# Performance work log

Hardware: AMD Instinct MI355X
Metric: run time of the kernel (lower is better)

## Reference

```python
import jax, jax.numpy as jnp
import numpy as np

EPS = 1e-3  # keras BatchNormalization epsilon=0.001
CLIP = 20.0

def bn(x, g, b, m, v):
    # inference-mode batch norm over last axis
    return (x - m) * jax.lax.rsqrt(v + EPS) * g + b

def conv1d_relu(x, w, b, stride):
    # x: [B,T,C], w: [K,Cin,Cout], VALID padding, relu
    y = jax.lax.conv_general_dilated(x, w, (stride,), 'VALID',
                                     dimension_numbers=('NWC', 'WIO', 'NWC'))
    return jax.nn.relu(y + b)

def gru_dir(xp, Wh, bh, reverse):
    # xp: [B,T,3H] precomputed input projection (x@Wx + input bias)
    # keras GRU, reset_after=True, activation=relu, recurrent_activation=sigmoid
    B, T, H3 = xp.shape
    H = H3 // 3
    def step(h, xt):
        mh = h @ Wh + bh                       # [B,3H]
        xz, xr, xh = jnp.split(xt, 3, axis=-1)
        rz, rr, rh = jnp.split(mh, 3, axis=-1)
        z = jax.nn.sigmoid(xz + rz)
        r = jax.nn.sigmoid(xr + rr)
        hh = jax.nn.relu(xh + r * rh)
        h = z * h + (1.0 - z) * hh
        return h, h
    xs = jnp.swapaxes(xp, 0, 1)                # [T,B,3H]
    h0 = jnp.zeros((B, H), xp.dtype)
    _, ys = jax.lax.scan(step, h0, xs, reverse=reverse)
    return jnp.swapaxes(ys, 0, 1)              # [B,T,H]

def bi_gru_sum(x, Wx, Wh, b):
    # Wx: [2,in,3H], Wh: [2,H,3H], b: [2,2,3H] (input bias, recurrent bias)
    out = None
    for d in range(2):
        xp = x @ Wx[d] + b[d, 0]
        y = gru_dir(xp, Wh[d], b[d, 1], reverse=(d == 1))
        out = y if out is None else out + y
    return out


def setup_inputs() -> dict:
    key = jax.random.key(0)
    ks = jax.random.split(key, 16)
    B, T, F = 16, 1600, 80
    C = 512      # conv filters / gru units / fc units
    K = 5        # kernel size
    L = 3        # bi_gru layers
    V = 6000     # output_dim
    def rn(k, shape, s):
        return (jax.random.normal(k, shape, jnp.float32) * s)
    inp = {
        'x': rn(ks[0], (B, T, F), 1.0),
        'bn1_g': jnp.ones((F,), jnp.float32), 'bn1_b': jnp.zeros((F,), jnp.float32),
        'bn1_m': rn(ks[1], (F,), 0.1), 'bn1_v': jnp.ones((F,), jnp.float32),
        'conv_w0': rn(ks[2], (K, F, C), 0.05), 'conv_b0': jnp.zeros((C,), jnp.float32),
        'conv_w1': rn(ks[3], (K, C, C), 0.02), 'conv_b1': jnp.zeros((C,), jnp.float32),
        'bn2_g': jnp.ones((C,), jnp.float32), 'bn2_b': jnp.zeros((C,), jnp.float32),
        'bn2_m': rn(ks[4], (C,), 0.1), 'bn2_v': jnp.ones((C,), jnp.float32),
        # stacked GRU params: [layers, 2 dirs, ...]; relu recurrence -> small init
        'gru_wx': rn(ks[5], (L, 2, C, 3 * C), 0.03),
        'gru_wh': rn(ks[6], (L, 2, C, 3 * C), 0.03),
        'gru_b': jnp.zeros((L, 2, 2, 3 * C), jnp.float32),
        'bn3_g': jnp.ones((C,), jnp.float32), 'bn3_b': jnp.zeros((C,), jnp.float32),
        'bn3_m': rn(ks[7], (C,), 0.1), 'bn3_v': jnp.ones((C,), jnp.float32),
        'fc_w': rn(ks[8], (C, C), 0.04), 'fc_b': jnp.zeros((C,), jnp.float32),
        'sm_w': rn(ks[9], (C, V), 0.04), 'sm_b': jnp.zeros((V,), jnp.float32),
    }
    return inp


def reference(x, bn1_g, bn1_b, bn1_m, bn1_v,
              conv_w0, conv_b0, conv_w1, conv_b1,
              bn2_g, bn2_b, bn2_m, bn2_v,
              gru_wx, gru_wh, gru_b,
              bn3_g, bn3_b, bn3_m, bn3_v,
              fc_w, fc_b, sm_w, sm_b):
    x = bn(x, bn1_g, bn1_b, bn1_m, bn1_v)
    x = conv1d_relu(x, conv_w0, conv_b0, 2)    # [B,798,512]
    x = conv1d_relu(x, conv_w1, conv_b1, 2)    # [B,397,512]
    x = bn(x, bn2_g, bn2_b, bn2_m, bn2_v)
    for l in range(gru_wx.shape[0]):
        x = bi_gru_sum(x, gru_wx[l], gru_wh[l], gru_b[l])
    x = bn(x, bn3_g, bn3_b, bn3_m, bn3_v)
    x = jnp.minimum(jax.nn.relu(x @ fc_w + fc_b), CLIP)  # clipped_relu(max=20)
    return jax.nn.softmax(x @ sm_w + sm_b, axis=-1)      # [B,397,6000]
```

## Files before the change

### kernel.cpp

```cpp
#include <hip/hip_runtime.h>
#include <math.h>

using bf16x8 = __attribute__((ext_vector_type(8))) short;
using f32x4  = __attribute__((ext_vector_type(4))) float;
using u32x4  = __attribute__((ext_vector_type(4))) unsigned int;
typedef unsigned short u16;
typedef unsigned int   u32;

#define EPSBN 1e-3f

__device__ __forceinline__ u16 f2bf(float f){
  union { float f; u32 u; } c; c.f = f;
  u32 u = c.u + 0x7fffu + ((c.u >> 16) & 1u);
  return (u16)(u >> 16);
}
__device__ __forceinline__ float bf2f(u16 b){
  union { u32 u; float f; } c; c.u = ((u32)b) << 16; return c.f;
}
__device__ __forceinline__ void splitstore(float v, u16* ph, u16* pl){
  u16 h = f2bf(v); *ph = h; *pl = f2bf(v - bf2f(h));
}
__device__ __forceinline__ f32x4 MFMA(bf16x8 a, bf16x8 b, f32x4 c){
  return __builtin_amdgcn_mfma_f32_16x16x32_bf16(a, b, c, 0, 0, 0);
}
__device__ __forceinline__ void glds16(const u16* g, u16* l){
  __builtin_amdgcn_global_load_lds(
      (const __attribute__((address_space(1))) void*)g,
      (__attribute__((address_space(3))) void*)l, 16, 0, 0);
}

__device__ __forceinline__ void st32_sys(u32* p, u32 v){
  asm volatile("global_store_dword %0, %1, off sc0 sc1" :: "v"(p), "v"(v) : "memory");
}
__device__ __forceinline__ u32 ld32_sys(const u32* p){
  u32 r;
  asm volatile("global_load_dword %0, %1, off sc0 sc1\n\ts_waitcnt vmcnt(0)"
               : "=v"(r) : "v"(p) : "memory");
  return r;
}

__global__ __launch_bounds__(256) void k_bn1_split(
    const float* __restrict__ x, const float* __restrict__ g, const float* __restrict__ b,
    const float* __restrict__ m, const float* __restrict__ v,
    u16* __restrict__ oh, u16* __restrict__ ol)
{
  int i = blockIdx.x*256 + threadIdx.x;
  if (i >= 2048000) return;
  int ci = i % 80;
  float s = g[ci] * rsqrtf(v[ci] + EPSBN);
  float val = (x[i] - m[ci]) * s + b[ci];
  splitstore(val, oh+i, ol+i);
}

__global__ __launch_bounds__(256) void k_prep_c1w(
    const float* __restrict__ w0, u16* __restrict__ oh, u16* __restrict__ ol)
{
  int i = blockIdx.x*256 + threadIdx.x;
  if (i >= 512*416) return;
  int co = i / 416, kf = i - co*416;
  float val = 0.f;
  if (kf < 400){ int kw = kf/80, ci = kf - kw*80; val = w0[(kw*80+ci)*512 + co]; }
  splitstore(val, oh+i, ol+i);
}

__global__ __launch_bounds__(256) void k_prep_c2w(
    const float* __restrict__ w1, u16* __restrict__ oh, u16* __restrict__ ol)
{
  int i = blockIdx.x*256 + threadIdx.x;
  if (i >= 5*512*512) return;
  int co = i & 511, ci = (i >> 9) & 511, kw = i >> 18;
  long o = (long)co*2560 + kw*512 + ci;
  splitstore(w1[i], oh+o, ol+o);
}

__global__ __launch_bounds__(256) void k_prep_wx(
    const float* __restrict__ wx, const float* __restrict__ g2, const float* __restrict__ v2,
    u16* __restrict__ oh, u16* __restrict__ ol)
{
  long i = (long)blockIdx.x*256 + threadIdx.x;
  if (i >= 6L*512*1536) return;
  int n = (int)(i % 1536); long r2 = i / 1536; int k = (int)(r2 % 512); int ld = (int)(r2 / 512);
  float s = (ld < 2) ? g2[k]*rsqrtf(v2[k]+EPSBN) : 1.f;
  long o = ((long)ld*1536 + n)*512 + k;
  splitstore(wx[i]*s, oh+o, ol+o);
}

__global__ __launch_bounds__(256) void k_prep_wh(
    const float* __restrict__ wh, u16* __restrict__ oh, u16* __restrict__ ol)
{
  long i = (long)blockIdx.x*256 + threadIdx.x;
  if (i >= 6L*512*1536) return;
  int n = (int)(i % 1536); long r2 = i / 1536; int k = (int)(r2 % 512); int ld = (int)(r2 / 512);
  long o = ((long)ld*1536 + n)*512 + k;
  splitstore(wh[i], oh+o, ol+o);
}

__global__ __launch_bounds__(256) void k_prep_grub(
    const float* __restrict__ gb, const float* __restrict__ wx,
    const float* __restrict__ g2, const float* __restrict__ b2,
    const float* __restrict__ m2, const float* __restrict__ v2,
    float* __restrict__ xbias, float* __restrict__ hbias)
{
  int i = blockIdx.x*256 + threadIdx.x;
  if (i >= 6*1536) return;
  int n = i % 1536, ld = i / 1536;
  float xv = gb[(ld*2 + 0)*1536 + n];
  float hv = gb[(ld*2 + 1)*1536 + n];
  if (ld < 2){
    float acc = 0.f;
    for (int k = 0; k < 512; ++k){
      float s = g2[k]*rsqrtf(v2[k]+EPSBN);
      float t = b2[k] - m2[k]*s;
      acc += t * wx[((long)ld*512 + k)*1536 + n];
    }
    xv += acc;
  }
  xbias[i] = xv; hbias[i] = hv;
}

__global__ __launch_bounds__(256) void k_prep_fcw(
    const float* __restrict__ fw, const float* __restrict__ g3, const float* __restrict__ v3,
    u16* __restrict__ oh, u16* __restrict__ ol)
{
  int i = blockIdx.x*256 + threadIdx.x;
  if (i >= 512*512) return;
  int n = i & 511, k = i >> 9;
  float s = g3[k]*rsqrtf(v3[k]+EPSBN);
  long o = (long)n*512 + k;
  splitstore(fw[i]*s, oh+o, ol+o);
}

__global__ __launch_bounds__(256) void k_prep_fcb(
    const float* __restrict__ fw, const float* __restrict__ fb,
    const float* __restrict__ g3, const float* __restrict__ b3,
    const float* __restrict__ m3, const float* __restrict__ v3,
    float* __restrict__ ob)
{
  int n = blockIdx.x*256 + threadIdx.x;
  if (n >= 512) return;
  float acc = fb[n];
  for (int k = 0; k < 512; ++k){
    float s = g3[k]*rsqrtf(v3[k]+EPSBN);
    float t = b3[k] - m3[k]*s;
    acc += t * fw[k*512 + n];
  }
  ob[n] = acc;
}

__global__ __launch_bounds__(256) void k_prep_smw(
    const float* __restrict__ sw, u16* __restrict__ oh, u16* __restrict__ ol)
{
  long i = (long)blockIdx.x*256 + threadIdx.x;
  if (i >= 512L*6000) return;
  int n = (int)(i % 6000); int k = (int)(i / 6000);
  long o = (long)n*512 + k;
  splitstore(sw[i], oh+o, ol+o);
}

__global__ __launch_bounds__(256) void k_sumsplit(
    const float* __restrict__ a, const float* __restrict__ b,
    u16* __restrict__ oh, u16* __restrict__ ol)
{
  int i = blockIdx.x*256 + threadIdx.x;
  if (i >= 6352*512) return;
  splitstore(a[i] + b[i], oh+i, ol+i);
}

template<int AMODE, int EPI>
__global__ __launch_bounds__(256,1)
void gemm_split(const u16* __restrict__ Ah, const u16* __restrict__ Al,
                const u16* __restrict__ Bh, const u16* __restrict__ Bl,
                const float* __restrict__ bias,
                float* __restrict__ outF, u16* __restrict__ outH, u16* __restrict__ outL,
                int M, int N, int K, int Kvalid, int TIN, int TOUT, int NYB)
{
  constexpr int CW = (AMODE==1) ? 80 : 512;
  const int tid  = threadIdx.x;
  const int lane = tid & 63;
  const int w    = tid >> 6;
  const int wm = w >> 1, wn = w & 1;
  const int r  = lane & 15, kg = lane >> 4;

  const int nwg = gridDim.x;
  const int q   = nwg >> 3;
  const int bid = blockIdx.x;
  const int wg  = (bid & 7) * q + (bid >> 3);
  const int bx  = wg / NYB, by = wg - bx * NYB;

  const int m0 = by * 64 + wm * 32;
  const int n0 = bx * 64 + wn * 32;

  long abase[2];
  #pragma unroll
  for (int mt = 0; mt < 2; ++mt){
    int m = m0 + mt*16 + r;
    int mc = m < M ? m : M - 1;
    if (AMODE == 0) abase[mt] = (long)mc * K;
    else { int bb = mc / TOUT; int tt = mc - bb * TOUT; abase[mt] = ((long)bb * TIN + 2*tt) * CW; }
  }
  long bbase[2];
  #pragma unroll
  for (int nt = 0; nt < 2; ++nt){
    int n = n0 + nt*16 + r;
    int nc = n < N ? n : N - 1;
    bbase[nt] = (long)nc * K;
  }

  f32x4 acc[2][2];
  #pragma unroll
  for (int a_ = 0; a_ < 2; ++a_)
    #pragma unroll
    for (int b_ = 0; b_ < 2; ++b_) acc[a_][b_] = f32x4{0.f,0.f,0.f,0.f};

  const bf16x8 zfrag = {0,0,0,0,0,0,0,0};
  const int koff = kg * 8;
  const int KT = K >> 5;
  for (int kt = 0; kt < KT; ++kt){
    int kf = kt*32 + koff;
    bf16x8 ah[2], al[2], bh[2], bl[2];
    #pragma unroll
    for (int nt = 0; nt < 2; ++nt){
      bh[nt] = *(const bf16x8*)(Bh + bbase[nt] + kf);
      bl[nt] = *(const bf16x8*)(Bl + bbase[nt] + kf);
    }
    #pragma unroll
    for (int mt = 0; mt < 2; ++mt){
      if (kf < Kvalid){
        int kw = kf / CW; int ci = kf - kw*CW;
        long ao = abase[mt] + (long)kw*CW + ci;
        ah[mt] = *(const bf16x8*)(Ah + ao); al[mt] = *(const bf16x8*)(Al + ao);
      } else { ah[mt] = zfrag; al[mt] = zfrag; }
    }
    #pragma unroll
    for (int mt = 0; mt < 2; ++mt)
      #pragma unroll
      for (int nt = 0; nt < 2; ++nt){
        acc[mt][nt] = MFMA(ah[mt], bh[nt], acc[mt][nt]);
        acc[mt][nt] = MFMA(ah[mt], bl[nt], acc[mt][nt]);
        acc[mt][nt] = MFMA(al[mt], bh[nt], acc[mt][nt]);
      }
  }

  #pragma unroll
  for (int nt = 0; nt < 2; ++nt){
    int n = n0 + nt*16 + r;
    if (n >= N) continue;
    float bv = bias ? bias[n] : 0.f;
    #pragma unroll
    for (int mt = 0; mt < 2; ++mt){
      #pragma unroll
      for (int q2 = 0; q2 < 4; ++q2){
        int m = m0 + mt*16 + kg*4 + q2;
        if (m >= M) continue;
        float v = acc[mt][nt][q2] + bv;
        if (EPI == 1) v = fmaxf(v, 0.f);
        if (EPI == 2) v = fminf(fmaxf(v, 0.f), 20.f);
        long o = (long)m * N + n;
        if (EPI == 0) outF[o] = v;
        else { u16 h = f2bf(v); outH[o] = h; outL[o] = f2bf(v - bf2f(h)); }
      }
    }
  }
}

template<int AMODE, int EPI>
__global__ __launch_bounds__(256,1)
void gemm_lds(const u16* __restrict__ Ah, const u16* __restrict__ Al,
              const u16* __restrict__ Bh, const u16* __restrict__ Bl,
              const float* __restrict__ bias,
              float* __restrict__ outF, u16* __restrict__ outH, u16* __restrict__ outL,
              int M, int N, int K, int TIN, int TOUT, int NYB, int NTILES)
{
  __shared__ __align__(16) u16 sAh[128*32], sAl[128*32], sBh[128*32], sBl[128*32];

  const int tid  = threadIdx.x;
  const int lane = tid & 63;
  const int w    = tid >> 6;
  const int wm = w >> 1, wn = w & 1;
  const int r  = lane & 15, kg = lane >> 4;

  const int nwg = gridDim.x;
  const int qq  = nwg >> 3;
  const int wg  = (blockIdx.x & 7) * qq + (blockIdx.x >> 3);
  if (wg >= NTILES) return;
  const int bx  = wg / NYB, by = wg - bx * NYB;
  const int m0 = by * 128, n0 = bx * 128;

  long aoff[2], boff[2]; int cbase[2];
  #pragma unroll
  for (int cc = 0; cc < 2; ++cc){
    int c = w*2 + cc;
    int li = c*64 + lane;
    int row = li >> 2, seg = li & 3;
    cbase[cc] = c*512;
    int ma = m0 + row; if (ma >= M) ma = M - 1;
    if (AMODE == 0) aoff[cc] = (long)ma * K + seg*8;
    else { int bb = ma / TOUT; int tt = ma - bb*TOUT;
           aoff[cc] = ((long)bb * TIN + 2*tt) * 512 + seg*8; }
    int nb = n0 + row; if (nb >= N) nb = N - 1;
    boff[cc] = (long)nb * K + seg*8;
  }

  int ard[4], brd[4];
  #pragma unroll
  for (int t4 = 0; t4 < 4; ++t4){
    ard[t4] = (wm*64 + t4*16 + r)*32 + kg*8;
    brd[t4] = (wn*64 + t4*16 + r)*32 + kg*8;
  }

  f32x4 acc[4][4];
  #pragma unroll
  for (int i = 0; i < 4; ++i)
    #pragma unroll
    for (int j = 0; j < 4; ++j) acc[i][j] = f32x4{0.f,0.f,0.f,0.f};

  const int KT = K >> 5;
  for (int kt = 0; kt < KT; ++kt){
    const long k32 = (long)kt*32;
    #pragma unroll
    for (int cc = 0; cc < 2; ++cc){
      glds16(Ah + aoff[cc] + k32, sAh + cbase[cc]);
      glds16(Al + aoff[cc] + k32, sAl + cbase[cc]);
      glds16(Bh + boff[cc] + k32, sBh + cbase[cc]);
      glds16(Bl + boff[cc] + k32, sBl + cbase[cc]);
    }
    asm volatile("s_waitcnt vmcnt(0)" ::: "memory");
    __syncthreads();

    bf16x8 ah[4], al[4], bh[4], bl[4];
    #pragma unroll
    for (int t4 = 0; t4 < 4; ++t4){
      ah[t4] = *(const bf16x8*)(sAh + ard[t4]);
      al[t4] = *(const bf16x8*)(sAl + ard[t4]);
      bh[t4] = *(const bf16x8*)(sBh + brd[t4]);
      bl[t4] = *(const bf16x8*)(sBl + brd[t4]);
    }
    #pragma unroll
    for (int i = 0; i < 4; ++i)
      #pragma unroll
      for (int j = 0; j < 4; ++j){
        acc[i][j] = MFMA(ah[i], bh[j], acc[i][j]);
        acc[i][j] = MFMA(ah[i], bl[j], acc[i][j]);
        acc[i][j] = MFMA(al[i], bh[j], acc[i][j]);
      }
    __syncthreads();
  }

  #pragma unroll
  for (int j = 0; j < 4; ++j){
    int n = n0 + wn*64 + j*16 + r;
    if (n >= N) continue;
    float bv = bias ? bias[n] : 0.f;
    #pragma unroll
    for (int i = 0; i < 4; ++i){
      #pragma unroll
      for (int q2 = 0; q2 < 4; ++q2){
        int m = m0 + wm*64 + i*16 + kg*4 + q2;
        if (m >= M) continue;
        float v = acc[i][j][q2] + bv;
        if (EPI == 1) v = fmaxf(v, 0.f);
        if (EPI == 2) v = fminf(fmaxf(v, 0.f), 20.f);
        long o = (long)m * N + n;
        if (EPI == 0) outF[o] = v;
        else { u16 h = f2bf(v); outH[o] = h; outL[o] = f2bf(v - bf2f(h)); }
      }
    }
  }
}

__global__ __launch_bounds__(256,1)
void gru_layer(const float* __restrict__ xp,
               const u16* __restrict__ WhH, const u16* __restrict__ WhL,
               const float* __restrict__ hbias,
               float* __restrict__ yf, float* __restrict__ yb,
               u32* __restrict__ hq,
               u32* __restrict__ flags,
               u32 lcode)
{
  const int dir = blockIdx.x >> 5;
  const int s   = blockIdx.x & 31;
  const int tid = threadIdx.x, lane = tid & 63, w = tid >> 6;
  const int r = lane & 15, kg = lane >> 4;

  const float* xpd = xp + (long)dir * (6352L*1536);
  const u16* whh = WhH + (long)dir * (1536L*512);
  const u16* whl = WhL + (long)dir * (1536L*512);
  const float* hb = hbias + dir * 1536;
  float* y = dir ? yb : yf;
  u32* flg = flags + dir * 512;

  __shared__ float red[2][4][3][64][4];

  bf16x8 Bh[3][4], Bl[3][4];
  #pragma unroll
  for (int g = 0; g < 3; ++g){
    long nb = (long)(g*512 + s*16 + r) * 512;
    #pragma unroll
    for (int kk = 0; kk < 4; ++kk){
      int k = (w*4 + kk)*32 + kg*8;
      Bh[g][kk] = *(const bf16x8*)(whh + nb + k);
      Bl[g][kk] = *(const bf16x8*)(whl + nb + k);
    }
  }

  const int gb = tid >> 4, gj = tid & 15;
  const int gcol = s*16 + gj;
  const float bz = hb[gcol], br = hb[512 + gcol], bhh = hb[1024 + gcol];
  const int rl = ((gb >> 2) << 4) | gj;
  const int rq = gb & 3;
  float hreg = 0.f;

  for (int t = 0; t < 397; ++t){
    const int tpos = dir ? (396 - t) : t;
    const long xb_ = ((long)gb*397 + tpos)*1536 + gcol;
    float xz = xpd[xb_], xr = xpd[xb_ + 512], xh = xpd[xb_ + 1024];

    f32x4 a0 = f32x4{0.f,0.f,0.f,0.f}, a1 = a0, a2 = a0;
    if (t > 0){
      if (w == 0){
        const u32 tgt = lcode + (u32)t;
        for (;;){
          int done = 1;
          if (lane < 32) done = (ld32_sys(flg + lane*16) >= tgt);
          if (__all(done)) break;
        }
      }
      __syncthreads();

      const u32* hqs = hq + ((long)t*2 + dir) * 8192;
      const int cbase2 = r*512 + kg*8;
      u32x4 q0[4], q1[4];
      #pragma unroll
      for (int kk = 0; kk < 4; ++kk){
        const u32x4* pp = (const u32x4*)(hqs + cbase2 + (w*4 + kk)*32);
        q0[kk] = pp[0]; q1[kk] = pp[1];
      }

      bf16x8 ah[4], al[4];
      #pragma unroll
      for (int kk = 0; kk < 4; ++kk){
        union { bf16x8 v; u32 u[4]; } A, L;
        A.u[0] = __builtin_amdgcn_perm(q0[kk].y, q0[kk].x, 0x07060302u);
        L.u[0] = __builtin_amdgcn_perm(q0[kk].y, q0[kk].x, 0x05040100u);
        A.u[1] = __builtin_amdgcn_perm(q0[kk].w, q0[kk].z, 0x07060302u);
        L.u[1] = __builtin_amdgcn_perm(q0[kk].w, q0[kk].z, 0x05040100u);
        A.u[2] = __builtin_amdgcn_perm(q1[kk].y, q1[kk].x, 0x07060302u);
        L.u[2] = __builtin_amdgcn_perm(q1[kk].y, q1[kk].x, 0x05040100u);
        A.u[3] = __builtin_amdgcn_perm(q1[kk].w, q1[kk].z, 0x07060302u);
        L.u[3] = __builtin_amdgcn_perm(q1[kk].w, q1[kk].z, 0x05040100u);
        ah[kk] = A.v; al[kk] = L.v;
      }
      #pragma unroll
      for (int kk = 0; kk < 4; ++kk){
        a0 = MFMA(ah[kk], Bh[0][kk], a0); a0 = MFMA(ah[kk], Bl[0][kk], a0); a0 = MFMA(al[kk], Bh[0][kk], a0);
        a1 = MFMA(ah[kk], Bh[1][kk], a1); a1 = MFMA(ah[kk], Bl[1][kk], a1); a1 = MFMA(al[kk], Bh[1][kk], a1);
        a2 = MFMA(ah[kk], Bh[2][kk], a2); a2 = MFMA(ah[kk], Bl[2][kk], a2); a2 = MFMA(al[kk], Bh[2][kk], a2);
      }
    }
    const int tb = t & 1;
    *(f32x4*)&red[tb][w][0][lane][0] = a0;
    *(f32x4*)&red[tb][w][1][lane][0] = a1;
    *(f32x4*)&red[tb][w][2][lane][0] = a2;
    __syncthreads();
    float rz = bz, rr = br, rh = bhh;
    #pragma unroll
    for (int ww = 0; ww < 4; ++ww){
      rz += red[tb][ww][0][rl][rq];
      rr += red[tb][ww][1][rl][rq];
      rh += red[tb][ww][2][rl][rq];
    }
    float z  = 1.f / (1.f + __expf(-(xz + rz)));
    float rg = 1.f / (1.f + __expf(-(xr + rr)));
    float hh = fmaxf(xh + rg * rh, 0.f);
    hreg = z * hreg + (1.f - z) * hh;

    {
      u32* o = hq + ((long)(t+1)*2 + dir) * 8192 + gb*512 + gcol;
      u16 hi = f2bf(hreg); u16 lo = f2bf(hreg - bf2f(hi));
      st32_sys(o, ((u32)hi << 16) | (u32)lo);
    }
    asm volatile("s_waitcnt vmcnt(0)" ::: "memory");
    __syncthreads();
    if (tid == 0) st32_sys(flg + s*16, lcode + (u32)(t + 1));
    y[((long)gb*397 + tpos)*512 + gcol] = hreg;
  }
}

__global__ __launch_bounds__(256,1) void k_softmax(float* __restrict__ out)
{
  const int tid = threadIdx.x;
  float* prow = out + (long)blockIdx.x * 6000;
  float vals[24];
  float mx = -3.0e38f;
  #pragma unroll
  for (int i = 0; i < 24; ++i){
    int idx = tid + i*256;
    vals[i] = (idx < 6000) ? prow[idx] : -3.0e38f;
    mx = fmaxf(mx, vals[i]);
  }
  #pragma unroll
  for (int o = 32; o; o >>= 1) mx = fmaxf(mx, __shfl_xor(mx, o));
  __shared__ float sred[4];
  if ((tid & 63) == 0) sred[tid >> 6] = mx;
  __syncthreads();
  mx = fmaxf(fmaxf(sred[0], sred[1]), fmaxf(sred[2], sred[3]));
  __syncthreads();
  float sum = 0.f;
  #pragma unroll
  for (int i = 0; i < 24; ++i){
    int idx = tid + i*256;
    vals[i] = (idx < 6000) ? expf(vals[i] - mx) : 0.f;
    sum += vals[i];
  }
  #pragma unroll
  for (int o = 32; o; o >>= 1) sum += __shfl_xor(sum, o);
  if ((tid & 63) == 0) sred[tid >> 6] = sum;
  __syncthreads();
  sum = sred[0] + sred[1] + sred[2] + sred[3];
  float inv = 1.f / sum;
  #pragma unroll
  for (int i = 0; i < 24; ++i){
    int idx = tid + i*256;
    if (idx < 6000) prow[idx] = vals[i] * inv;
  }
}

extern "C" void kernel_launch(void* const* d_in, const int* in_sizes, int n_in,
                              void* d_out, int out_size, void* d_ws, size_t ws_size,
                              hipStream_t stream)
{
  (void)in_sizes; (void)n_in; (void)out_size; (void)ws_size;
  const float* x    = (const float*)d_in[0];
  const float* bn1g = (const float*)d_in[1];
  const float* bn1b = (const float*)d_in[2];
  const float* bn1m = (const float*)d_in[3];
  const float* bn1v = (const float*)d_in[4];
  const float* cw0  = (const float*)d_in[5];
  const float* cb0  = (const float*)d_in[6];
  const float* cw1  = (const float*)d_in[7];
  const float* cb1  = (const float*)d_in[8];
  const float* bn2g = (const float*)d_in[9];
  const float* bn2b = (const float*)d_in[10];
  const float* bn2m = (const float*)d_in[11];
  const float* bn2v = (const float*)d_in[12];
  const float* gwx  = (const float*)d_in[13];
  const float* gwh  = (const float*)d_in[14];
  const float* gbia = (const float*)d_in[15];
  const float* bn3g = (const float*)d_in[16];
  const float* bn3b = (const float*)d_in[17];
  const float* bn3m = (const float*)d_in[18];
  const float* bn3v = (const float*)d_in[19];
  const float* fcw  = (const float*)d_in[20];
  const float* fcb  = (const float*)d_in[21];
  const float* smw  = (const float*)d_in[22];
  const float* smb  = (const float*)d_in[23];

  char* p = (char*)d_ws;
  auto alloc = [&](size_t bytes)->char*{
    char* q = p; p += (bytes + 255) & ~(size_t)255; return q;
  };
  const size_t NX=2048000, NC1W=512*416, NC1O=12768L*512, NC2W=512*2560,
               NC2O=6352L*512, NWX=6L*1536*512, NXP=2L*6352*1536,
               NSMW=6000L*512, NFCW=512*512;

  u16 *xbnH=(u16*)alloc(NX*2),  *xbnL=(u16*)alloc(NX*2);
  u16 *c1wH=(u16*)alloc(NC1W*2),*c1wL=(u16*)alloc(NC1W*2);
  u16 *c1oH=(u16*)alloc(NC1O*2),*c1oL=(u16*)alloc(NC1O*2);
  u16 *c2wH=(u16*)alloc(NC2W*2),*c2wL=(u16*)alloc(NC2W*2);
  u16 *c2oH=(u16*)alloc(NC2O*2),*c2oL=(u16*)alloc(NC2O*2);
  u16 *wxH=(u16*)alloc(NWX*2),  *wxL=(u16*)alloc(NWX*2);
  u16 *whH=(u16*)alloc(NWX*2),  *whL=(u16*)alloc(NWX*2);
  float *xbias=(float*)alloc(6*1536*4), *hbias=(float*)alloc(6*1536*4);
  float *xp=(float*)alloc(NXP*4);
  float *yf=(float*)alloc(NC2O*4), *yb=(float*)alloc(NC2O*4);
  u16 *ysH=(u16*)alloc(NC2O*2), *ysL=(u16*)alloc(NC2O*2);
  u16 *fcwH=(u16*)alloc(NFCW*2),*fcwL=(u16*)alloc(NFCW*2);
  float *fcb2=(float*)alloc(512*4);
  u16 *fcoH=(u16*)alloc(NC2O*2),*fcoL=(u16*)alloc(NC2O*2);
  u16 *smwH=(u16*)alloc(NSMW*2),*smwL=(u16*)alloc(NSMW*2);
  u32 *hq=(u32*)alloc(398L*2*8192*4);
  u32 *flags=(u32*)alloc(2*512*4);

  hipMemsetAsync(flags, 0, 2*512*4, stream);

  k_bn1_split<<<8000,256,0,stream>>>(x, bn1g,bn1b,bn1m,bn1v, xbnH,xbnL);
  k_prep_c1w <<<832,256,0,stream>>>(cw0, c1wH,c1wL);
  k_prep_c2w <<<5120,256,0,stream>>>(cw1, c2wH,c2wL);
  k_prep_wx  <<<18432,256,0,stream>>>(gwx, bn2g,bn2v, wxH,wxL);
  k_prep_wh  <<<18432,256,0,stream>>>(gwh, whH,whL);
  k_prep_grub<<<36,256,0,stream>>>(gbia, gwx, bn2g,bn2b,bn2m,bn2v, xbias,hbias);
  k_prep_fcw <<<1024,256,0,stream>>>(fcw, bn3g,bn3v, fcwH,fcwL);
  k_prep_fcb <<<2,256,0,stream>>>(fcw,fcb, bn3g,bn3b,bn3m,bn3v, fcb2);
  k_prep_smw <<<12000,256,0,stream>>>(smw, smwH,smwL);

  gemm_split<1,1><<<1600,256,0,stream>>>(xbnH,xbnL, c1wH,c1wL, cb0,
      nullptr, c1oH,c1oL, 12768,512,416, 400, 1600,798, 200);
  gemm_lds<2,1><<<200,256,0,stream>>>(c1oH,c1oL, c2wH,c2wL, cb1,
      nullptr, c2oH,c2oL, 6352,512,2560, 798,397, 50, 200);

  const u16 *aH = c2oH, *aL = c2oL;
  for (int l = 0; l < 3; ++l){
    for (int d = 0; d < 2; ++d){
      gemm_lds<0,0><<<600,256,0,stream>>>(aH,aL,
          wxH + (size_t)(l*2+d)*786432, wxL + (size_t)(l*2+d)*786432,
          xbias + (l*2+d)*1536,
          xp + (size_t)d*9756672, nullptr,nullptr,
          6352,1536,512, 0,0, 50, 600);
    }
    gru_layer<<<64,256,0,stream>>>(xp,
        whH + (size_t)l*2*786432, whL + (size_t)l*2*786432,
        hbias + l*2*1536, yf,yb, hq, flags, (u32)((l+1)*1000));
    k_sumsplit<<<12704,256,0,stream>>>(yf,yb, ysH,ysL);
    aH = ysH; aL = ysL;
  }

  gemm_lds<0,2><<<200,256,0,stream>>>(ysH,ysL, fcwH,fcwL, fcb2,
      nullptr, fcoH,fcoL, 6352,512,512, 0,0, 50, 200);
  gemm_lds<0,0><<<2352,256,0,stream>>>(fcoH,fcoL, smwH,smwL, smb,
      (float*)d_out, nullptr,nullptr, 6352,6000,512, 0,0, 50, 2350);
  k_softmax<<<6352,256,0,stream>>>((float*)d_out);
}
```

Baseline: 4.971 ms.

## Use LDS-tiled GEMM for conv1 and merge both GRU direction projections

Removes the register-only gemm_split kernel and runs the first strided conv through the LDS-tiled GEMM, templated on channel width (80 for conv1, 512 for conv2). The two per-direction input-projection GEMMs of each GRU layer become one GEMM with N=3072, writing an interleaved [rows,3072] xp buffer, and the GRU kernel indexing is changed to match. Launch bounds also go to 2 blocks per CU. The aim is better operand reuse, fewer launches and higher occupancy. The risks are register pressure under the tighter bound and conv1's K=416 (13 tiles of 32) meeting the CW=80 window addressing.

```diff
diff --git a/kernel.cpp b/kernel.cpp
--- a/kernel.cpp
+++ b/kernel.cpp
@@ -166,105 +166,8 @@
   splitstore(a[i] + b[i], oh+i, ol+i);
 }
 
-template<int AMODE, int EPI>
-__global__ __launch_bounds__(256,1)
-void gemm_split(const u16* __restrict__ Ah, const u16* __restrict__ Al,
-                const u16* __restrict__ Bh, const u16* __restrict__ Bl,
-                const float* __restrict__ bias,
-                float* __restrict__ outF, u16* __restrict__ outH, u16* __restrict__ outL,
-                int M, int N, int K, int Kvalid, int TIN, int TOUT, int NYB)
-{
-  constexpr int CW = (AMODE==1) ? 80 : 512;
-  const int tid  = threadIdx.x;
-  const int lane = tid & 63;
-  const int w    = tid >> 6;
-  const int wm = w >> 1, wn = w & 1;
-  const int r  = lane & 15, kg = lane >> 4;
-
-  const int nwg = gridDim.x;
-  const int q   = nwg >> 3;
-  const int bid = blockIdx.x;
-  const int wg  = (bid & 7) * q + (bid >> 3);
-  const int bx  = wg / NYB, by = wg - bx * NYB;
-
-  const int m0 = by * 64 + wm * 32;
-  const int n0 = bx * 64 + wn * 32;
-
-  long abase[2];
-  #pragma unroll
-  for (int mt = 0; mt < 2; ++mt){
-    int m = m0 + mt*16 + r;
-    int mc = m < M ? m : M - 1;
-    if (AMODE == 0) abase[mt] = (long)mc * K;
-    else { int bb = mc / TOUT; int tt = mc - bb * TOUT; abase[mt] = ((long)bb * TIN + 2*tt) * CW; }
-  }
-  long bbase[2];
-  #pragma unroll
-  for (int nt = 0; nt < 2; ++nt){
-    int n = n0 + nt*16 + r;
-    int nc = n < N ? n : N - 1;
-    bbase[nt] = (long)nc * K;
-  }
-
-  f32x4 acc[2][2];
-  #pragma unroll
-  for (int a_ = 0; a_ < 2; ++a_)
-    #pragma unroll
-    for (int b_ = 0; b_ < 2; ++b_) acc[a_][b_] = f32x4{0.f,0.f,0.f,0.f};
-
-  const bf16x8 zfrag = {0,0,0,0,0,0,0,0};
-  const int koff = kg * 8;
-  const int KT = K >> 5;
-  for (int kt = 0; kt < KT; ++kt){
-    int kf = kt*32 + koff;
-    bf16x8 ah[2], al[2], bh[2], bl[2];
-    #pragma unroll
-    for (int nt = 0; nt < 2; ++nt){
-      bh[nt] = *(const bf16x8*)(Bh + bbase[nt] + kf);
-      bl[nt] = *(const bf16x8*)(Bl + bbase[nt] + kf);
-    }
-    #pragma unroll
-    for (int mt = 0; mt < 2; ++mt){
-      if (kf < Kvalid){
-        int kw = kf / CW; int ci = kf - kw*CW;
-        long ao = abase[mt] + (long)kw*CW + ci;
-        ah[mt] = *(const bf16x8*)(Ah + ao); al[mt] = *(const bf16x8*)(Al + ao);
-      } else { ah[mt] = zfrag; al[mt] = zfrag; }
-    }
-    #pragma unroll
-    for (int mt = 0; mt < 2; ++mt)
-      #pragma unroll
-      for (int nt = 0; nt < 2; ++nt){
-        acc[mt][nt] = MFMA(ah[mt], bh[nt], acc[mt][nt]);
-        acc[mt][nt] = MFMA(ah[mt], bl[nt], acc[mt][nt]);
-        acc[mt][nt] = MFMA(al[mt], bh[nt], acc[mt][nt]);
-      }
-  }
-
-  #pragma unroll
-  for (int nt = 0; nt < 2; ++nt){
-    int n = n0 + nt*16 + r;
-    if (n >= N) continue;
-    float bv = bias ? bias[n] : 0.f;
-    #pragma unroll
-    for (int mt = 0; mt < 2; ++mt){
-      #pragma unroll
-      for (int q2 = 0; q2 < 4; ++q2){
-        int m = m0 + mt*16 + kg*4 + q2;
-        if (m >= M) continue;
-        float v = acc[mt][nt][q2] + bv;
-        if (EPI == 1) v = fmaxf(v, 0.f);
-        if (EPI == 2) v = fminf(fmaxf(v, 0.f), 20.f);
-        long o = (long)m * N + n;
-        if (EPI == 0) outF[o] = v;
-        else { u16 h = f2bf(v); outH[o] = h; outL[o] = f2bf(v - bf2f(h)); }
-      }
-    }
-  }
-}
-
-template<int AMODE, int EPI>
-__global__ __launch_bounds__(256,1)
+template<int CW, int EPI>
+__global__ __launch_bounds__(256,2)
 void gemm_lds(const u16* __restrict__ Ah, const u16* __restrict__ Al,
               const u16* __restrict__ Bh, const u16* __restrict__ Bl,
               const float* __restrict__ bias,
@@ -294,9 +197,9 @@
     int row = li >> 2, seg = li & 3;
     cbase[cc] = c*512;
     int ma = m0 + row; if (ma >= M) ma = M - 1;
-    if (AMODE == 0) aoff[cc] = (long)ma * K + seg*8;
+    if (CW == 0) aoff[cc] = (long)ma * K + seg*8;
     else { int bb = ma / TOUT; int tt = ma - bb*TOUT;
-           aoff[cc] = ((long)bb * TIN + 2*tt) * 512 + seg*8; }
+           aoff[cc] = ((long)bb * TIN + 2*tt) * CW + seg*8; }
     int nb = n0 + row; if (nb >= N) nb = N - 1;
     boff[cc] = (long)nb * K + seg*8;
   }
@@ -382,7 +285,7 @@
   const int tid = threadIdx.x, lane = tid & 63, w = tid >> 6;
   const int r = lane & 15, kg = lane >> 4;
 
-  const float* xpd = xp + (long)dir * (6352L*1536);
+  const float* xpd = xp + dir * 1536;
   const u16* whh = WhH + (long)dir * (1536L*512);
   const u16* whl = WhL + (long)dir * (1536L*512);
   const float* hb = hbias + dir * 1536;
@@ -412,7 +315,7 @@
 
   for (int t = 0; t < 397; ++t){
     const int tpos = dir ? (396 - t) : t;
-    const long xb_ = ((long)gb*397 + tpos)*1536 + gcol;
+    const long xb_ = ((long)gb*397 + tpos)*3072 + gcol;
     float xz = xpd[xb_], xr = xpd[xb_ + 512], xh = xpd[xb_ + 1024];
 
     f32x4 a0 = f32x4{0.f,0.f,0.f,0.f}, a1 = a0, a2 = a0;
@@ -560,7 +463,7 @@
     char* q = p; p += (bytes + 255) & ~(size_t)255; return q;
   };
   const size_t NX=2048000, NC1W=512*416, NC1O=12768L*512, NC2W=512*2560,
-               NC2O=6352L*512, NWX=6L*1536*512, NXP=2L*6352*1536,
+               NC2O=6352L*512, NWX=6L*1536*512, NXP=6352L*3072,
                NSMW=6000L*512, NFCW=512*512;
 
   u16 *xbnH=(u16*)alloc(NX*2),  *xbnL=(u16*)alloc(NX*2);
@@ -593,20 +496,18 @@
   k_prep_fcb <<<2,256,0,stream>>>(fcw,fcb, bn3g,bn3b,bn3m,bn3v, fcb2);
   k_prep_smw <<<12000,256,0,stream>>>(smw, smwH,smwL);
 
-  gemm_split<1,1><<<1600,256,0,stream>>>(xbnH,xbnL, c1wH,c1wL, cb0,
-      nullptr, c1oH,c1oL, 12768,512,416, 400, 1600,798, 200);
-  gemm_lds<2,1><<<200,256,0,stream>>>(c1oH,c1oL, c2wH,c2wL, cb1,
+  gemm_lds<80,1><<<400,256,0,stream>>>(xbnH,xbnL, c1wH,c1wL, cb0,
+      nullptr, c1oH,c1oL, 12768,512,416, 1600,798, 100, 400);
+  gemm_lds<512,1><<<200,256,0,stream>>>(c1oH,c1oL, c2wH,c2wL, cb1,
       nullptr, c2oH,c2oL, 6352,512,2560, 798,397, 50, 200);
 
   const u16 *aH = c2oH, *aL = c2oL;
   for (int l = 0; l < 3; ++l){
-    for (int d = 0; d < 2; ++d){
-      gemm_lds<0,0><<<600,256,0,stream>>>(aH,aL,
-          wxH + (size_t)(l*2+d)*786432, wxL + (size_t)(l*2+d)*786432,
-          xbias + (l*2+d)*1536,
-          xp + (size_t)d*9756672, nullptr,nullptr,
-          6352,1536,512, 0,0, 50, 600);
-    }
+    gemm_lds<0,0><<<1200,256,0,stream>>>(aH,aL,
+        wxH + (size_t)l*2*786432, wxL + (size_t)l*2*786432,
+        xbias + (size_t)l*3072,
+        xp, nullptr,nullptr,
+        6352,3072,512, 0,0, 50, 1200);
     gru_layer<<<64,256,0,stream>>>(xp,
         whH + (size_t)l*2*786432, whL + (size_t)l*2*786432,
         hbias + l*2*1536, yf,yb, hq, flags, (u32)((l+1)*1000));
```

New measurement: 4.796 ms. 1.04x faster.
